# Optimization experiments

Measured on AMD Instinct MI355X. Metric: run time of the kernel, lower is better.

The kernel has to match this reference:

```python
import jax, jax.numpy as jnp
import numpy as np
from jax import lax

B, NQ, C = 2, 1024, 2048
H, DH = 16, 128
G, CD = 4, 512          # off_grps, off_dim = C // G
LR, HR = 24, 72         # low-res grid side, high-res grid side
INTER = 64
K = LR * LR             # sampled K/V tokens (grid_size == lr_size)


def setup_inputs() -> dict:
    key = jax.random.key(0)
    ks = jax.random.split(key, 16)
    s = 0.02
    d = {}
    d['hidden_states'] = jax.random.normal(ks[0], (B, NQ, C), jnp.float32)
    d['image_hd'] = jax.random.normal(ks[1], (B, HR * HR, C), jnp.float32)
    d['wq'] = jax.random.normal(ks[2], (C, C), jnp.float32) * s
    d['wk'] = jax.random.normal(ks[3], (C, C), jnp.float32) * s
    d['wv'] = jax.random.normal(ks[4], (C, C), jnp.float32) * s
    d['wo'] = jax.random.normal(ks[5], (C, C), jnp.float32) * s
    d['conv_dw_w'] = jax.random.normal(ks[6], (CD, 1, 3, 3), jnp.float32) * s
    d['ln1_w'] = jnp.ones((CD,), jnp.float32)
    d['ln1_b'] = jnp.zeros((CD,), jnp.float32)
    d['conv_lr_proj_w'] = jax.random.normal(ks[7], (INTER, CD), jnp.float32) * s
    d['proj_int_w'] = jax.random.normal(ks[8], (INTER, CD), jnp.float32) * s
    d['proj_int_b'] = jnp.zeros((INTER,), jnp.float32)
    d['ln2_w'] = jnp.ones((INTER,), jnp.float32)
    d['ln2_b'] = jnp.zeros((INTER,), jnp.float32)
    d['conv_off_w'] = jax.random.normal(ks[9], (2, INTER), jnp.float32) * s
    d['k_hd_w'] = jax.random.normal(ks[10], (C, C), jnp.float32) * s
    d['k_hd_b'] = jnp.zeros((C,), jnp.float32)
    d['v_hd_w'] = jax.random.normal(ks[11], (C, C), jnp.float32) * s
    d['v_hd_b'] = jnp.zeros((C,), jnp.float32)
    return d


def _ln_channels(x, w, b, eps=1e-5):
    # LayerNorm2d: normalize over channel axis of [N, C, H, W]
    mu = jnp.mean(x, axis=1, keepdims=True)
    var = jnp.var(x, axis=1, keepdims=True)
    xn = (x - mu) * lax.rsqrt(var + eps)
    return xn * w[None, :, None, None] + b[None, :, None, None]


def _tokens_to_grid(x, S):
    # [B, S*S, C] -> [B*G, CD, S, S]  (group channels like einops '(b) (h w) (g c) -> (b g) c h w')
    return x.reshape(B, S, S, G, CD).transpose(0, 3, 4, 1, 2).reshape(B * G, CD, S, S)


def _bilinear_sample(img, grid):
    # img [N, C, Hh, Wh]; grid [N, K, 2] (x, y) normalized to [-1, 1], align_corners=True
    N, Cc, Hh, Wh = img.shape
    x = (grid[..., 0] + 1.0) * 0.5 * (Wh - 1)
    y = (grid[..., 1] + 1.0) * 0.5 * (Hh - 1)
    x0f, y0f = jnp.floor(x), jnp.floor(y)
    wx = (x - x0f)[:, None, :]
    wy = (y - y0f)[:, None, :]
    x0 = jnp.clip(x0f.astype(jnp.int32), 0, Wh - 1)
    x1 = jnp.clip(x0 + 1, 0, Wh - 1)
    y0 = jnp.clip(y0f.astype(jnp.int32), 0, Hh - 1)
    y1 = jnp.clip(y0 + 1, 0, Hh - 1)
    imgf = img.reshape(N, Cc, Hh * Wh)
    gather = jax.vmap(lambda im, ix: im[:, ix])  # ([C,HW],[K]) -> [C,K]
    v00 = gather(imgf, y0 * Wh + x0)
    v01 = gather(imgf, y0 * Wh + x1)
    v10 = gather(imgf, y1 * Wh + x0)
    v11 = gather(imgf, y1 * Wh + x1)
    return (v00 * (1 - wx) * (1 - wy) + v01 * wx * (1 - wy)
            + v10 * (1 - wx) * wy + v11 * wx * wy)  # [N, C, K]


def _ref_grid():
    # normalized reference points as in _grid_generate (centers / (S-1) * 2 - 1)
    yy = (jnp.linspace(0.5, LR - 0.5, LR) / (LR - 1.0)) * 2.0 - 1.0
    xx = (jnp.linspace(0.5, LR - 0.5, LR) / (LR - 1.0)) * 2.0 - 1.0
    gy, gx = jnp.meshgrid(yy, xx, indexing='ij')
    return jnp.stack([gx, gy], axis=-1).reshape(K, 2)  # (x, y)


def reference(hidden_states, image_hd, wq, wk, wv, wo, conv_dw_w, ln1_w, ln1_b,
              conv_lr_proj_w, proj_int_w, proj_int_b, ln2_w, ln2_b, conv_off_w,
              k_hd_w, k_hd_b, v_hd_w, v_hd_b):
    # ---- QKV on the full sequence ----
    q = hidden_states @ wq.T
    k_txt = hidden_states @ wk.T
    v_txt = hidden_states @ wv.T

    # ---- offset network on LR image tokens (first LR*LR tokens) ----
    lr = _tokens_to_grid(hidden_states[:, :K, :], LR)          # [B*G, CD, LR, LR]
    x = lax.conv_general_dilated(lr, conv_dw_w, (1, 1), 'SAME',
                                 feature_group_count=CD,
                                 dimension_numbers=('NCHW', 'OIHW', 'NCHW'))
    x = jax.nn.silu(x)
    x = _ln_channels(x, ln1_w, ln1_b)
    x = jnp.einsum('nchw,oc->nohw', x, conv_lr_proj_w)          # 1x1 conv -> [B*G, INTER, LR, LR]
    # intention gate from spatially pooled group features
    pooled = jnp.mean(lr, axis=(2, 3))                          # [B*G, CD]
    gate = jax.nn.sigmoid(pooled @ proj_int_w.T + proj_int_b)   # [B*G, INTER]
    x = x * gate[:, :, None, None]
    x = _ln_channels(x, ln2_w, ln2_b)
    off = jnp.einsum('nchw,oc->nohw', x, conv_off_w)            # [B*G, 2, LR, LR]
    off = off.transpose(0, 2, 3, 1).reshape(B * G, K, 2)        # (x, y)
    pos = jnp.tanh(_ref_grid()[None] + off)                     # sampling locs in [-1, 1]

    # ---- deformable gather from HD features ----
    hd = _tokens_to_grid(image_hd, HR)                          # [B*G, CD, HR, HR]
    samp = _bilinear_sample(hd, pos)                            # [B*G, CD, K]
    samp = samp.reshape(B, G, CD, K).transpose(0, 3, 1, 2).reshape(B, K, C)
    k_hd = samp @ k_hd_w.T + k_hd_b
    v_hd = samp @ v_hd_w.T + v_hd_b

    # ---- attention: causal over text tokens, HD tokens fully visible ----
    k_all = jnp.concatenate([k_txt, k_hd], axis=1)              # [B, NQ+K, C]
    v_all = jnp.concatenate([v_txt, v_hd], axis=1)
    qh = q.reshape(B, NQ, H, DH).transpose(0, 2, 1, 3)
    kh = k_all.reshape(B, NQ + K, H, DH).transpose(0, 2, 1, 3)
    vh = v_all.reshape(B, NQ + K, H, DH).transpose(0, 2, 1, 3)
    scores = jnp.einsum('bhqd,bhkd->bhqk', qh, kh) / jnp.sqrt(jnp.float32(DH))
    col = jnp.arange(NQ + K)
    row = jnp.arange(NQ)
    allow = (col[None, :] >= NQ) | (col[None, :] <= row[:, None])
    scores = jnp.where(allow[None, None], scores, jnp.float32(-1e9))
    attn = jax.nn.softmax(scores, axis=-1)
    out = jnp.einsum('bhqk,bhkd->bhqd', attn, vh)
    out = out.transpose(0, 2, 1, 3).reshape(B, NQ, C)
    return out @ wo.T
```

## Files before the change

kernel.cpp:

```cpp
#include <hip/hip_runtime.h>

typedef unsigned short u16;
typedef unsigned int u32;
typedef __attribute__((ext_vector_type(8))) short bf8;
typedef __attribute__((ext_vector_type(4))) float f4;
typedef __attribute__((ext_vector_type(4))) unsigned short us4;

constexpr int B = 2;
constexpr int NQ = 1024;
constexpr int C = 2048;
constexpr int DH = 128;
constexpr int G = 4;
constexpr int CD = 512;
constexpr int LR = 24;
constexpr int HR = 72;
constexpr int INTER = 64;
constexpr int K = LR * LR;
constexpr int NKV = NQ + K;

#define MFMA16(a, b, c) __builtin_amdgcn_mfma_f32_16x16x32_bf16(a, b, c, 0, 0, 0)
#define GLDS(g, l)                                                         \
  __builtin_amdgcn_global_load_lds(                                        \
      (const __attribute__((address_space(1))) void*)(g),                  \
      (__attribute__((address_space(3))) void*)(l), 16, 0, 0)
#define SB()                               \
  do {                                     \
    __builtin_amdgcn_sched_barrier(0);     \
    __builtin_amdgcn_s_barrier();          \
    __builtin_amdgcn_sched_barrier(0);     \
  } while (0)
#define WVM(n)                                              \
  do {                                                      \
    asm volatile("s_waitcnt vmcnt(" #n ")" ::: "memory");   \
    __builtin_amdgcn_sched_barrier(0);                      \
  } while (0)

__device__ __forceinline__ u16 f2bf1(float f) {
  u32 u = __float_as_uint(f);
  u32 r = (u + 0x7fffu + ((u >> 16) & 1u)) >> 16;
  return (u16)r;
}

__global__ __launch_bounds__(256) void f2bf_k9b(
    const float* __restrict__ s0, const float* __restrict__ s1,
    const float* __restrict__ s2, const float* __restrict__ s3,
    const float* __restrict__ s4, const float* __restrict__ s5,
    const float* __restrict__ s6, const float* __restrict__ plrw,
    const float* __restrict__ cdw, u16* __restrict__ d0, u16* __restrict__ d1,
    u16* __restrict__ d2, u16* __restrict__ d3, u16* __restrict__ d4,
    u16* __restrict__ d5, u16* __restrict__ d6, float* __restrict__ wt,
    float* __restrict__ x1, float* __restrict__ pooled) {
  __shared__ float SH[16 * 577];
  const int y = blockIdx.y;
  const int t = threadIdx.x;
  if (y == 7) {
    if (blockIdx.x >= 128) return;
    const int idx = blockIdx.x * 256 + t;
    wt[idx] = plrw[(idx & 63) * 512 + (idx >> 6)];
    return;
  }
  if (y == 8) {
    if (blockIdx.x >= 256) return;
    const int n = blockIdx.x >> 5, cg = blockIdx.x & 31;
    const int b = n >> 2, g = n & 3;
    const int c0 = cg * 16;
    {
      const int c = t & 15, pr = t >> 4;
      const float* src = s0 + (size_t)b * 1024 * 2048 + g * 512 + c0 + c;
#pragma unroll 4
      for (int j = 0; j < 36; ++j) {
        const int p = j * 16 + pr;
        SH[c * 577 + p] = src[(size_t)p * 2048];
      }
    }
    __syncthreads();
    {
      const int c = t >> 4, seg = t & 15;
      float s = 0.f;
      for (int i = 0; i < 36; ++i) s += SH[c * 577 + seg * 36 + i];
      s += __shfl_xor(s, 1);
      s += __shfl_xor(s, 2);
      s += __shfl_xor(s, 4);
      s += __shfl_xor(s, 8);
      if (seg == 0) pooled[n * 512 + c0 + c] = s * (1.f / 576.f);
    }
    const size_t base_out = (size_t)(n * 512 + c0) * 576;
    for (int j = 0; j < 36; ++j) {
      const int idx = j * 256 + t;
      const int c = idx / 576, p = idx - c * 576;
      const int yy0 = p / 24, xx0 = p - yy0 * 24;
      const float* wp = cdw + (c0 + c) * 9;
      float s = 0.f;
#pragma unroll
      for (int dy = -1; dy <= 1; ++dy)
#pragma unroll
        for (int dx = -1; dx <= 1; ++dx) {
          const int yy = yy0 + dy, xx = xx0 + dx;
          if (yy < 0 || yy >= 24 || xx < 0 || xx >= 24) continue;
          s += SH[c * 577 + yy * 24 + xx] * wp[(dy + 1) * 3 + dx + 1];
        }
      x1[base_out + idx] = s / (1.f + expf(-s));
    }
    return;
  }
  const float* s;
  u16* d;
  switch (y) {
    case 0: s = s0; d = d0; break;
    case 1: s = s1; d = d1; break;
    case 2: s = s2; d = d2; break;
    case 3: s = s3; d = d3; break;
    case 4: s = s4; d = d4; break;
    case 5: s = s5; d = d5; break;
    default: s = s6; d = d6; break;
  }
  u16* L = (u16*)SH;
  const int pc = blockIdx.x;
  const int mb = pc >> 5, kb = pc & 31;
  const int rin = t >> 2, c0 = (t & 3) * 16;
  const float* src = s + (size_t)(mb * 64 + rin) * 2048 + kb * 64 + c0;
#pragma unroll
  for (int j = 0; j < 16; j += 4) {
    float4 v = *(const float4*)(src + j);
    L[rin * 68 + c0 + j] = f2bf1(v.x);
    L[rin * 68 + c0 + j + 1] = f2bf1(v.y);
    L[rin * 68 + c0 + j + 2] = f2bf1(v.z);
    L[rin * 68 + c0 + j + 3] = f2bf1(v.w);
  }
  __syncthreads();
  u16* dst = d + (size_t)pc * 4096 + t * 16;
#pragma unroll
  for (int gg = 0; gg < 2; ++gg) {
    const int g = t * 2 + gg;
    const int rh = g & 15, ks2 = (g >> 4) & 3, kc = (g >> 6) & 1, fr = g >> 7;
    const int row = fr * 16 + rh, cc = kc * 32 + ks2 * 8;
    us4 o0, o1;
    o0.x = L[row * 68 + cc];     o0.y = L[row * 68 + cc + 1];
    o0.z = L[row * 68 + cc + 2]; o0.w = L[row * 68 + cc + 3];
    o1.x = L[row * 68 + cc + 4]; o1.y = L[row * 68 + cc + 5];
    o1.z = L[row * 68 + cc + 6]; o1.w = L[row * 68 + cc + 7];
    *(us4*)(dst + gg * 8) = o0;
    *(us4*)(dst + gg * 8 + 4) = o1;
  }
}

__global__ __launch_bounds__(512, 2) void gemm_qkv_hd(
    const u16* __restrict__ Ast, const u16* __restrict__ Wq,
    const u16* __restrict__ Wk, const u16* __restrict__ Wv,
    const u16* __restrict__ sampst, const u16* __restrict__ khwst,
    const u16* __restrict__ vhwst, const float* __restrict__ khb,
    const float* __restrict__ vhb, u16* __restrict__ outq,
    u16* __restrict__ kg, u16* __restrict__ vg) {
  __shared__ u16 As[2][4][4096];
  __shared__ u16 Bs[2][4][4096];
  const int tid = threadIdx.x, lane = tid & 63, w = tid >> 6;
  const int ks = lane >> 4, r = lane & 15;
  const int bid = blockIdx.x;

  if (bid < 192) {
    const int wm = w >> 2, wn = w & 3;
    const int swz = (bid & 7) * 24 + (bid >> 3);
    const int mt = swz / 24, nt = swz % 24;
    const u16* Wst = (nt < 8) ? Wq : (nt < 16) ? Wk : Wv;
    const int nb0 = (nt & 7) * 4;
    const int mb0 = mt * 4;

#define ST_A03(bi, kt)                                                        \
  do {                                                                        \
    GLDS(Ast + ((size_t)(mb0 + 0) * 32 + (kt)) * 4096 + tid * 8,              \
         &As[bi][0][tid * 8]);                                                \
    GLDS(Ast + ((size_t)(mb0 + 2) * 32 + (kt)) * 4096 + tid * 8,              \
         &As[bi][2][tid * 8]);                                                \
  } while (0)
#define ST_A47(bi, kt)                                                        \
  do {                                                                        \
    GLDS(Ast + ((size_t)(mb0 + 1) * 32 + (kt)) * 4096 + tid * 8,              \
         &As[bi][1][tid * 8]);                                                \
    GLDS(Ast + ((size_t)(mb0 + 3) * 32 + (kt)) * 4096 + tid * 8,              \
         &As[bi][3][tid * 8]);                                                \
  } while (0)
#define ST_B01(bi, kt)                                                        \
  do {                                                                        \
    GLDS(Wst + ((size_t)(nb0 + 0) * 32 + (kt)) * 4096 + tid * 8,              \
         &Bs[bi][0][tid * 8]);                                                \
    GLDS(Wst + ((size_t)(nb0 + 1) * 32 + (kt)) * 4096 + tid * 8,              \
         &Bs[bi][1][tid * 8]);                                                \
  } while (0)
#define ST_B23(bi, kt)                                                        \
  do {                                                                        \
    GLDS(Wst + ((size_t)(nb0 + 2) * 32 + (kt)) * 4096 + tid * 8,              \
         &Bs[bi][2][tid * 8]);                                                \
    GLDS(Wst + ((size_t)(nb0 + 3) * 32 + (kt)) * 4096 + tid * 8,              \
         &Bs[bi][3][tid * 8]);                                                \
  } while (0)
#define RD_A(dst, bi, half, kc)                                               \
  _Pragma("unroll") for (int i2 = 0; i2 < 4; ++i2) dst[i2] =                  \
      *(const bf8*)(&As[bi][wm * 2 + (half)]                                  \
                       [((i2 * 2 + (kc)) * 4 + ks) * 128 + r * 8]);
#define RD_B(dst, bi, kc)                                                     \
  _Pragma("unroll") for (int j2 = 0; j2 < 4; ++j2) dst[j2] =                  \
      *(const bf8*)(&Bs[bi][wn][((j2 * 2 + (kc)) * 4 + ks) * 128 + r * 8]);
#define MM(ACC, AF, BF)                                                       \
  do {                                                                        \
    __builtin_amdgcn_s_setprio(1);                                            \
    _Pragma("unroll") for (int i3 = 0; i3 < 4; ++i3)                          \
        _Pragma("unroll") for (int j3 = 0; j3 < 4; ++j3) ACC[i3][j3] =        \
            MFMA16(AF[i3], BF[j3], ACC[i3][j3]);                              \
    __builtin_amdgcn_s_setprio(0);                                            \
  } while (0)

    f4 accA[4][4], accB[4][4];
#pragma unroll
    for (int i = 0; i < 4; ++i)
#pragma unroll
      for (int j = 0; j < 4; ++j) {
        accA[i][j] = f4{0.f, 0.f, 0.f, 0.f};
        accB[i][j] = f4{0.f, 0.f, 0.f, 0.f};
      }
    bf8 af[4], b0[4], b1[4];

    ST_A03(0, 0); ST_B01(0, 0); ST_B23(0, 0); ST_A47(0, 0);
    ST_A03(1, 1); ST_B01(1, 1);
    WVM(6);
    SB();

    for (int t = 0; t < 32; ++t) {
      const int buf = t & 1;
      RD_A(af, buf, 0, 0);
      RD_B(b0, buf, 0);
      if (t + 1 < 32) ST_B23(buf ^ 1, t + 1);
      SB();
      MM(accA, af, b0);
      SB();
      RD_A(af, buf, 0, 1);
      RD_B(b1, buf, 1);
      if (t + 1 < 32) ST_A47(buf ^ 1, t + 1);
      SB();
      MM(accA, af, b1);
      if (t + 1 < 32) { WVM(8); } else { WVM(0); }
      SB();
      RD_A(af, buf, 1, 0);
      if (t + 2 < 32) ST_A03(buf, t + 2);
      SB();
      MM(accB, af, b0);
      SB();
      RD_A(af, buf, 1, 1);
      if (t + 2 < 32) ST_B01(buf, t + 2);
      SB();
      MM(accB, af, b1);
      if (t + 2 < 32) { WVM(6); } else if (t + 1 < 32) { WVM(2); }
      SB();
    }

#define EPI(ACC, HALF)                                                        \
  _Pragma("unroll") for (int i = 0; i < 4; ++i)                               \
      _Pragma("unroll") for (int j = 0; j < 4; ++j)                           \
          _Pragma("unroll") for (int rr = 0; rr < 4; ++rr) {                  \
    const int m = mt * 256 + wm * 128 + (HALF)*64 + i * 16 + ks * 4 + rr;     \
    const int n = nt * 256 + wn * 64 + j * 16 + r;                            \
    const float v = ACC[i][j][rr];                                            \
    const int sel = n >> 11, nn = n & 2047, hh = nn >> 7, dd = nn & 127;      \
    const int bb = m >> 10, qq = m & 1023;                                    \
    const u16 bv = f2bf1(v);                                                  \
    if (sel == 0) {                                                           \
      outq[(size_t)m * 2048 + nn] = bv;                                       \
    } else if (sel == 1) {                                                    \
      kg[(((size_t)(bb * 16 + hh) * 50 + (qq >> 5)) * 16 + (dd >> 3)) * 256 + \
         (qq & 31) * 8 + (dd & 7)] = bv;                                      \
    } else {                                                                  \
      vg[((size_t)(bb * 16 + hh) * 200 + (qq >> 3)) * 1024 + dd * 8 +         \
         (qq & 7)] = bv;                                                      \
    }                                                                         \
  }
    EPI(accA, 0)
    EPI(accB, 1)
#undef EPI
  } else {
    u16* A3 = &As[0][0][0];
    u16* Bk3 = &As[0][0][0] + 12288;
    u16* Bv3 = &Bs[0][0][0];
    const int hb = bid - 192;
    const int mt = hb / 16, nt = hb % 16;
    const int ma0 = mt * 2, nb0 = nt * 2;
    const bool is_v = (w >= 4);
    const int wv4 = w & 3;
    const int wr = wv4 >> 1, wc = wv4 & 1;
    const u16* Wsrc = is_v ? vhwst : khwst;
    u16* Wdst = is_v ? Bv3 : Bk3;
    const u16* Brd = is_v ? Bv3 : Bk3;

#define HDST(bi, kt)                                                          \
  do {                                                                        \
    const int kb_ = (kt) >> 1, kc_ = (kt) & 1;                                \
    GLDS(sampst + ((size_t)(ma0 + (w >> 2)) * 32 + kb_) * 4096 +              \
             (w & 3) * 1024 + kc_ * 512 + lane * 8,                           \
         &A3[(bi)*4096 + w * 512 + lane * 8]);                                \
    _Pragma("unroll") for (int r2 = 0; r2 < 2; ++r2) {                        \
      const int run = r2 * 4 + wv4;                                           \
      GLDS(Wsrc + ((size_t)(nb0 + (run >> 2)) * 32 + kb_) * 4096 +            \
               (run & 3) * 1024 + kc_ * 512 + lane * 8,                       \
           &Wdst[(bi)*4096 + run * 512 + lane * 8]);                          \
    }                                                                         \
  } while (0)

    f4 acc[4][4];
#pragma unroll
    for (int i = 0; i < 4; ++i)
#pragma unroll
      for (int j = 0; j < 4; ++j) acc[i][j] = f4{0.f, 0.f, 0.f, 0.f};

    HDST(0, 0);
    HDST(1, 1);
    int rd = 0;
    for (int kt = 0; kt < 64; ++kt) {
      SB();
      if (kt + 2 < 64) {
        const int wb = (rd + 2 >= 3) ? rd - 1 : rd + 2;
        HDST(wb, kt + 2);
        WVM(6);
      } else if (kt + 1 < 64) {
        WVM(3);
      } else {
        WVM(0);
      }
      SB();
      bf8 af2[4], bw[4];
#pragma unroll
      for (int i = 0; i < 4; ++i)
        af2[i] =
            *(const bf8*)(&A3[rd * 4096 + (wr * 4 + i) * 512 + ks * 128 + r * 8]);
#pragma unroll
      for (int j = 0; j < 4; ++j)
        bw[j] =
            *(const bf8*)(&Brd[rd * 4096 + (wc * 4 + j) * 512 + ks * 128 + r * 8]);
      __builtin_amdgcn_s_setprio(1);
#pragma unroll
      for (int i = 0; i < 4; ++i)
#pragma unroll
        for (int j = 0; j < 4; ++j)
          acc[i][j] = MFMA16(af2[i], bw[j], acc[i][j]);
      __builtin_amdgcn_s_setprio(0);
      rd = (rd + 1 >= 3) ? 0 : rd + 1;
    }
#undef HDST
    const int rbase = ks * 4;
    const float* bias = is_v ? vhb : khb;
#pragma unroll
    for (int i = 0; i < 4; ++i)
#pragma unroll
      for (int j = 0; j < 4; ++j) {
        const int nn = nt * 128 + wc * 64 + j * 16 + r;
        const int hh = nn >> 7, dd = nn & 127;
#pragma unroll
        for (int rr = 0; rr < 4; ++rr) {
          const int m = mt * 128 + wr * 64 + i * 16 + rbase + rr;
          const int bb = m / 576;
          const int kv = 1024 + (m - bb * 576);
          const u16 bv = f2bf1(acc[i][j][rr] + bias[nn]);
          if (!is_v) {
            kg[(((size_t)(bb * 16 + hh) * 50 + (kv >> 5)) * 16 + (dd >> 3)) *
                   256 +
               (kv & 31) * 8 + (dd & 7)] = bv;
          } else {
            vg[((size_t)(bb * 16 + hh) * 200 + (kv >> 3)) * 1024 + dd * 8 +
               (kv & 7)] = bv;
          }
        }
      }
  }
}

__global__ __launch_bounds__(256) void gemm_out3(const u16* __restrict__ Ast,
                                                 const u16* __restrict__ W0,
                                                 float* __restrict__ outf) {
  __shared__ u16 As[3][4096];
  __shared__ u16 Bs[3][4096];
  const int tid = threadIdx.x, lane = tid & 63, w = tid >> 6;
  const int wr = w >> 1, wc = w & 1;
  const int ksl = lane >> 4, rl = lane & 15;
  const int xcd = blockIdx.x & 7, idx = blockIdx.x >> 3;
  const int mt = (xcd >> 2) * 8 + idx / 4;
  const int nt = (xcd & 3) * 4 + idx % 4;
  const u16* Wp = W0;
  const int ma0 = mt * 2;
  const int nb0 = nt * 2;

#define GST2(dstArr, srcBase, tb0, kt)                                     \
  do {                                                                     \
    const int kb_ = (kt) >> 1, kc_ = (kt) & 1;                             \
    _Pragma("unroll") for (int r2 = 0; r2 < 2; ++r2) {                     \
      const int run = r2 * 4 + w;                                          \
      GLDS(srcBase + ((size_t)((tb0) + (run >> 2)) * 32 + kb_) * 4096 +    \
               (run & 3) * 1024 + kc_ * 512 + lane * 8,                    \
           &dstArr[run * 512 + lane * 8]);                                 \
    }                                                                      \
  } while (0)

  f4 acc[4][4];
#pragma unroll
  for (int i = 0; i < 4; ++i)
#pragma unroll
    for (int j = 0; j < 4; ++j) acc[i][j] = f4{0.f, 0.f, 0.f, 0.f};

  GST2(As[0], Ast, ma0, 0);
  GST2(Bs[0], Wp, nb0, 0);
  GST2(As[1], Ast, ma0, 1);
  GST2(Bs[1], Wp, nb0, 1);
  int rd = 0;
  for (int kt = 0; kt < 64; ++kt) {
    SB();
    if (kt + 2 < 64) {
      const int wb = (rd + 2 >= 3) ? rd - 1 : rd + 2;
      GST2(As[wb], Ast, ma0, kt + 2);
      GST2(Bs[wb], Wp, nb0, kt + 2);
      WVM(8);
    } else if (kt + 1 < 64) {
      WVM(4);
    } else {
      WVM(0);
    }
    SB();
    bf8 af[4], bw[4];
#pragma unroll
    for (int i = 0; i < 4; ++i)
      af[i] = *(const bf8*)(&As[rd][(wr * 4 + i) * 512 + ksl * 128 + rl * 8]);
#pragma unroll
    for (int j = 0; j < 4; ++j)
      bw[j] = *(const bf8*)(&Bs[rd][(wc * 4 + j) * 512 + ksl * 128 + rl * 8]);
    __builtin_amdgcn_s_setprio(1);
#pragma unroll
    for (int i = 0; i < 4; ++i)
#pragma unroll
      for (int j = 0; j < 4; ++j)
        acc[i][j] = MFMA16(af[i], bw[j], acc[i][j]);
    __builtin_amdgcn_s_setprio(0);
    rd = (rd + 1 >= 3) ? 0 : rd + 1;
  }
#undef GST2

  const int rbase = ksl * 4;
#pragma unroll
  for (int i = 0; i < 4; ++i)
#pragma unroll
    for (int j = 0; j < 4; ++j) {
      const int n = nt * 128 + wc * 64 + j * 16 + rl;
#pragma unroll
      for (int rr = 0; rr < 4; ++rr) {
        const int m = mt * 128 + wr * 64 + i * 16 + rbase + rr;
        outf[(size_t)m * 2048 + n] = acc[i][j][rr];
      }
    }
}

__global__ __launch_bounds__(256) void lnproj_gate(
    const float* __restrict__ x1, const float* __restrict__ ln1w,
    const float* __restrict__ ln1b, const float* __restrict__ wt,
    const float* __restrict__ pooled, const float* __restrict__ piw,
    const float* __restrict__ pib, float* __restrict__ x2,
    float* __restrict__ gate) {
  __shared__ float Xs[512][68];
  __shared__ float rs[4][64], rss[4][64];
  const int bidx = blockIdx.x;
  const int t = threadIdx.x;
  if (bidx >= 72) {
    const int idx = (bidx - 72) * 256 + t;
    const int n = idx >> 6, o = idx & 63;
    const float* pb = pooled + n * 512;
    const float* wb = piw + o * 512;
    float s = pib[o];
    for (int c = 0; c < 512; ++c) s += pb[c] * wb[c];
    gate[idx] = 1.f / (1.f + expf(-s));
    return;
  }
  const int n = bidx / 9, pc = bidx % 9;
  const int p0 = pc * 64;
  {
    const int pl = t & 63, c4 = t >> 6;
    const float* src = x1 + (size_t)n * 512 * 576 + p0 + pl;
#pragma unroll 4
    for (int j = 0; j < 128; ++j) {
      const int c = j * 4 + c4;
      Xs[c][pl] = src[(size_t)c * 576];
    }
  }
  __syncthreads();
  {
    const int pl = t & 63, q = t >> 6;
    float s = 0.f, ss = 0.f;
    for (int c = q * 128; c < q * 128 + 128; ++c) {
      const float v = Xs[c][pl];
      s += v;
      ss += v * v;
    }
    rs[q][pl] = s;
    rss[q][pl] = ss;
    __syncthreads();
    const float S = rs[0][pl] + rs[1][pl] + rs[2][pl] + rs[3][pl];
    const float SS = rss[0][pl] + rss[1][pl] + rss[2][pl] + rss[3][pl];
    const float mean = S * (1.f / 512.f);
    const float inv = rsqrtf(SS * (1.f / 512.f) - mean * mean + 1e-5f);
    for (int c = q * 128; c < q * 128 + 128; ++c)
      Xs[c][pl] = (Xs[c][pl] - mean) * inv * ln1w[c] + ln1b[c];
  }
  __syncthreads();
  {
    const int o4 = (t & 15) * 4, pl0 = (t >> 4) * 4;
    float acc[4][4] = {};
    for (int c = 0; c < 512; ++c) {
      const f4 xv = *(const f4*)(&Xs[c][pl0]);
      const f4 wv = *(const f4*)(&wt[c * 64 + o4]);
#pragma unroll
      for (int i = 0; i < 4; ++i)
#pragma unroll
        for (int j = 0; j < 4; ++j) acc[i][j] += wv[i] * xv[j];
    }
#pragma unroll
    for (int i = 0; i < 4; ++i) {
      f4 ov;
      ov[0] = acc[i][0]; ov[1] = acc[i][1];
      ov[2] = acc[i][2]; ov[3] = acc[i][3];
      *(f4*)(&x2[(size_t)(n * 64 + o4 + i) * 576 + p0 + pl0]) = ov;
    }
  }
}

__global__ __launch_bounds__(256) void pos_sample(
    const float* __restrict__ x2, const float* __restrict__ gate,
    const float* __restrict__ ln2w, const float* __restrict__ ln2b,
    const float* __restrict__ offw, const float* __restrict__ img,
    u16* __restrict__ sampst) {
  const int bk = blockIdx.x;
  const int b = bk / K, k = bk % K;
  __shared__ int s_idx[G][4];
  __shared__ float s_w[G][4];
  const int t = threadIdx.x;
  const int g = t >> 6, lane = t & 63;
  {
    const int n = b * G + g;
    float v = x2[((size_t)n * INTER + lane) * K + k] * gate[n * INTER + lane];
    float s = v, ss = v * v;
    for (int o = 32; o; o >>= 1) {
      s += __shfl_xor(s, o);
      ss += __shfl_xor(ss, o);
    }
    const float mean = s * (1.f / INTER);
    const float var = ss * (1.f / INTER) - mean * mean;
    const float xn = (v - mean) * rsqrtf(var + 1e-5f) * ln2w[lane] + ln2b[lane];
    float ox = xn * offw[lane];
    float oy = xn * offw[INTER + lane];
    for (int o = 32; o; o >>= 1) {
      ox += __shfl_xor(ox, o);
      oy += __shfl_xor(oy, o);
    }
    if (lane == 0) {
      const int yi = k / LR, xi = k % LR;
      const float rx = (xi + 0.5f) / 23.f * 2.f - 1.f;
      const float ry = (yi + 0.5f) / 23.f * 2.f - 1.f;
      const float px = tanhf(rx + ox), py = tanhf(ry + oy);
      const float x = (px + 1.f) * 0.5f * (HR - 1);
      const float y = (py + 1.f) * 0.5f * (HR - 1);
      const float x0f = floorf(x), y0f = floorf(y);
      const float wx = x - x0f, wy = y - y0f;
      const int x0 = min(max((int)x0f, 0), HR - 1);
      const int x1 = min(x0 + 1, HR - 1);
      const int y0 = min(max((int)y0f, 0), HR - 1);
      const int y1 = min(y0 + 1, HR - 1);
      s_idx[g][0] = y0 * HR + x0;
      s_idx[g][1] = y0 * HR + x1;
      s_idx[g][2] = y1 * HR + x0;
      s_idx[g][3] = y1 * HR + x1;
      s_w[g][0] = (1.f - wx) * (1.f - wy);
      s_w[g][1] = wx * (1.f - wy);
      s_w[g][2] = (1.f - wx) * wy;
      s_w[g][3] = wx * wy;
    }
  }
  __syncthreads();
  const int m = b * 576 + k;
  const int mb = m >> 6, fr = (m >> 4) & 3, r = m & 15;
  const int ch0 = t * 8;
  const int gg = ch0 >> 9;
  const float* ib = img + (size_t)b * HR * HR * C + ch0;
  float v[8];
#pragma unroll
  for (int j = 0; j < 8; ++j) v[j] = 0.f;
#pragma unroll
  for (int q = 0; q < 4; ++q) {
    const float wq_ = s_w[gg][q];
    const float* p = ib + (size_t)s_idx[gg][q] * C;
    const float4 a = *(const float4*)p;
    const float4 c = *(const float4*)(p + 4);
    v[0] += wq_ * a.x; v[1] += wq_ * a.y; v[2] += wq_ * a.z; v[3] += wq_ * a.w;
    v[4] += wq_ * c.x; v[5] += wq_ * c.y; v[6] += wq_ * c.z; v[7] += wq_ * c.w;
  }
  const int kb = ch0 >> 6, kc = (ch0 >> 5) & 1, ks3 = (ch0 >> 3) & 3;
  u16* dst = sampst + ((size_t)(mb * 32 + kb)) * 4096 +
             (((fr * 2 + kc) * 4 + ks3) * 16 + r) * 8;
  us4 o0, o1;
  o0.x = f2bf1(v[0]); o0.y = f2bf1(v[1]); o0.z = f2bf1(v[2]); o0.w = f2bf1(v[3]);
  o1.x = f2bf1(v[4]); o1.y = f2bf1(v[5]); o1.z = f2bf1(v[6]); o1.w = f2bf1(v[7]);
  *(us4*)dst = o0;
  *(us4*)(dst + 4) = o1;
}

__global__ __launch_bounds__(256) void attn_u(
    const u16* __restrict__ qb, const u16* __restrict__ kg,
    const u16* __restrict__ vg, u16* __restrict__ aob_st) {
  const int i = blockIdx.x;
  const int pair = i & 255, half = i >> 8;
  const int bh = pair & 31;
  const int q8 = pair >> 5;
  const int qblk = half ? (15 - q8) : q8;
  const int b = bh >> 4, h = bh & 15;
  const int q0 = qblk * 64;
  const int tid = threadIdx.x, lane = tid & 63, w = tid >> 6;
  const int qw = q0 + w * 16;
  const int col = lane & 15, kpart = lane >> 4, rbase = kpart * 4;
  __shared__ u16 Ks[2][4096];
  __shared__ u16 Vs[2][4096];
  __shared__ u16 Pl[4][16 * 40];
  bf8 qf[4];
  {
    const u16* qp =
        qb + (size_t)(b * 1024 + qw + col) * 2048 + h * 128 + kpart * 8;
#pragma unroll
    for (int dc = 0; dc < 4; ++dc) qf[dc] = *(const bf8*)(qp + dc * 32);
  }
  f4 o[8];
#pragma unroll
  for (int df = 0; df < 8; ++df) o[df] = f4{0.f, 0.f, 0.f, 0.f};
  float m_r[4] = {-1e30f, -1e30f, -1e30f, -1e30f};
  float l_p[4] = {0.f, 0.f, 0.f, 0.f};
  const float scale = 0.08838834764831845f;
  const int nt_text = (q0 + 64) >> 5;
  const int nt = nt_text + 18;
  const u16* kbh = kg + (size_t)bh * (NKV * 128);
  const u16* vbh = vg + (size_t)bh * (NKV * 128);
  u16* pw = &Pl[w][0];

#define ASTAGE(bi, kv0)                                                       \
  do {                                                                        \
    const u16* gk = kbh + (size_t)((kv0) >> 5) * 4096 + w * 1024 + lane * 8;  \
    GLDS(gk, &Ks[bi][w * 1024 + lane * 8]);                                   \
    GLDS(gk + 512, &Ks[bi][w * 1024 + 512 + lane * 8]);                       \
    const u16* gv = vbh + (size_t)((kv0) >> 3) * 1024 + w * 1024 + lane * 8;  \
    GLDS(gv, &Vs[bi][w * 1024 + lane * 8]);                                   \
    GLDS(gv + 512, &Vs[bi][w * 1024 + 512 + lane * 8]);                       \
  } while (0)

  ASTAGE(0, 0);
  int cur = 0;
  for (int t = 0; t < nt; ++t) {
    const bool is_text = t < nt_text;
    const int kv0 = is_text ? (t << 5) : (1024 + ((t - nt_text) << 5));
    SB();
    if (t + 1 < nt) {
      const int t1 = t + 1;
      const int kv1 =
          (t1 < nt_text) ? (t1 << 5) : (1024 + ((t1 - nt_text) << 5));
      ASTAGE(cur ^ 1, kv1);
      WVM(4);
    } else {
      WVM(0);
    }
    SB();
    const u16* ksb = &Ks[cur][0];
    const u16* vsb = &Vs[cur][0];
    f4 s0 = {0.f, 0.f, 0.f, 0.f}, s1 = {0.f, 0.f, 0.f, 0.f};
    __builtin_amdgcn_s_setprio(1);
#pragma unroll
    for (int dc = 0; dc < 4; ++dc) {
      const int dblk = dc * 4 + kpart;
      bf8 k0f = *(const bf8*)(ksb + (dblk * 32 + col) * 8);
      bf8 k1f = *(const bf8*)(ksb + (dblk * 32 + 16 + col) * 8);
      s0 = MFMA16(qf[dc], k0f, s0);
      s1 = MFMA16(qf[dc], k1f, s1);
    }
    __builtin_amdgcn_s_setprio(0);
    float sa[4], sc[4], loc[4], p0[4], p1[4];
    bool grow = false;
    const bool need_mask = is_text && (kv0 + 31 > qw);
#pragma unroll
    for (int rr = 0; rr < 4; ++rr) {
      float a = s0[rr] * scale, c2 = s1[rr] * scale;
      if (need_mask) {
        const int qg = qw + rbase + rr;
        if (kv0 + col > qg) a = -1e30f;
        if (kv0 + 16 + col > qg) c2 = -1e30f;
      }
      sa[rr] = a; sc[rr] = c2;
      loc[rr] = fmaxf(a, c2);
      grow |= (loc[rr] > m_r[rr] + 8.f);
    }
    if (__any(grow)) {
      float fr[4];
#pragma unroll
      for (int rr = 0; rr < 4; ++rr) {
        float mx = loc[rr];
        mx = fmaxf(mx, __shfl_xor(mx, 1));
        mx = fmaxf(mx, __shfl_xor(mx, 2));
        mx = fmaxf(mx, __shfl_xor(mx, 4));
        mx = fmaxf(mx, __shfl_xor(mx, 8));
        const float mn = fmaxf(m_r[rr], mx);
        fr[rr] = __expf(m_r[rr] - mn);
        m_r[rr] = mn;
        p0[rr] = __expf(sa[rr] - mn);
        p1[rr] = __expf(sc[rr] - mn);
        l_p[rr] = l_p[rr] * fr[rr] + p0[rr] + p1[rr];
      }
#pragma unroll
      for (int df = 0; df < 8; ++df) {
        o[df][0] *= fr[0]; o[df][1] *= fr[1];
        o[df][2] *= fr[2]; o[df][3] *= fr[3];
      }
    } else {
#pragma unroll
      for (int rr = 0; rr < 4; ++rr) {
        p0[rr] = __expf(sa[rr] - m_r[rr]);
        p1[rr] = __expf(sc[rr] - m_r[rr]);
        l_p[rr] += p0[rr] + p1[rr];
      }
    }
#pragma unroll
    for (int rr = 0; rr < 4; ++rr) {
      pw[(rbase + rr) * 40 + col] = f2bf1(p0[rr]);
      pw[(rbase + rr) * 40 + 16 + col] = f2bf1(p1[rr]);
    }
    bf8 pa = *(const bf8*)(pw + col * 40 + kpart * 8);
    __builtin_amdgcn_s_setprio(1);
#pragma unroll
    for (int df = 0; df < 8; ++df) {
      bf8 vf = *(const bf8*)(vsb + (kpart * 128 + df * 16 + col) * 8);
      o[df] = MFMA16(pa, vf, o[df]);
    }
    __builtin_amdgcn_s_setprio(0);
    cur ^= 1;
  }
#undef ASTAGE
  float inv[4];
#pragma unroll
  for (int rr = 0; rr < 4; ++rr) {
    float ps = l_p[rr];
    ps += __shfl_xor(ps, 1);
    ps += __shfl_xor(ps, 2);
    ps += __shfl_xor(ps, 4);
    ps += __shfl_xor(ps, 8);
    inv[rr] = 1.f / ps;
  }
#pragma unroll
  for (int rr = 0; rr < 4; ++rr) {
    const int m = b * 1024 + qw + rbase + rr;
    const int mb = m >> 6, fr3 = (m >> 4) & 3, r16 = m & 15;
#pragma unroll
    for (int df = 0; df < 8; ++df) {
      const int ncol = h * 128 + df * 16 + col;
      const int kb = ncol >> 6, kc = (ncol >> 5) & 1, ks3 = (ncol >> 3) & 3,
                j0 = ncol & 7;
      aob_st[((size_t)(mb * 32 + kb)) * 4096 +
             (((fr3 * 2 + kc) * 4 + ks3) * 16 + r16) * 8 + j0] =
          f2bf1(o[df][rr] * inv[rr]);
    }
  }
}

extern "C" void kernel_launch(void* const* d_in, const int* in_sizes, int n_in,
                              void* d_out, int out_size, void* d_ws,
                              size_t ws_size, hipStream_t stream) {
  const float* hs = (const float*)d_in[0];
  const float* img = (const float*)d_in[1];
  const float* wq = (const float*)d_in[2];
  const float* wk = (const float*)d_in[3];
  const float* wv = (const float*)d_in[4];
  const float* wo = (const float*)d_in[5];
  const float* cdw = (const float*)d_in[6];
  const float* ln1w = (const float*)d_in[7];
  const float* ln1b = (const float*)d_in[8];
  const float* plrw = (const float*)d_in[9];
  const float* piw = (const float*)d_in[10];
  const float* pib = (const float*)d_in[11];
  const float* ln2w = (const float*)d_in[12];
  const float* ln2b = (const float*)d_in[13];
  const float* offw = (const float*)d_in[14];
  const float* khw = (const float*)d_in[15];
  const float* khb = (const float*)d_in[16];
  const float* vhw = (const float*)d_in[17];
  const float* vhb = (const float*)d_in[18];
  float* outp = (float*)d_out;

  u16* wsp = (u16*)d_ws;
  const size_t SZ = 4194304;
  u16* hs_st = wsp;
  u16* wq_st = wsp + SZ;
  u16* wk_st = wsp + 2 * SZ;
  u16* wv_st = wsp + 3 * SZ;
  u16* wo_st = wsp + 4 * SZ;
  u16* khw_st = wsp + 5 * SZ;
  u16* vhw_st = wsp + 6 * SZ;
  u16* qb_bf = wsp + 7 * SZ;
  u16* samp_st = wsp + 8 * SZ;
  u16* kg = wsp + 8 * SZ + 2359296;
  u16* vg = kg + 6553600;
  float* x1b = (float*)kg + 2359296;
  float* x2b = x1b + 2359296;
  float* poolb = x2b + 294912;
  float* gb = poolb + 4096;
  float* wtb = (float*)(vg + 6553600);
  u16* aob_st = wq_st;

  dim3 blk(256);
  f2bf_k9b<<<dim3(1024, 9), blk, 0, stream>>>(
      hs, wq, wk, wv, wo, khw, vhw, plrw, cdw, hs_st, wq_st, wk_st, wv_st,
      wo_st, khw_st, vhw_st, wtb, x1b, poolb);
  lnproj_gate<<<dim3(74), blk, 0, stream>>>(x1b, ln1w, ln1b, wtb, poolb, piw,
                                            pib, x2b, gb);
  pos_sample<<<dim3(B * K), blk, 0, stream>>>(x2b, gb, ln2w, ln2b, offw, img,
                                              samp_st);
  gemm_qkv_hd<<<dim3(336), dim3(512), 0, stream>>>(
      hs_st, wq_st, wk_st, wv_st, samp_st, khw_st, vhw_st, khb, vhb, qb_bf,
      kg, vg);
  attn_u<<<dim3(512), blk, 0, stream>>>(qb_bf, kg, vg, aob_st);
  gemm_out3<<<dim3(256), blk, 0, stream>>>(aob_st, wo_st, outp);
}
```

Baseline: 338.0 us.

## Widen attention KV tile to 64 keys and reorder QKV/HD GEMM block dispatch

The attention kernel now processes 64 keys per pipeline step instead of 32. This halves the number of barrier and stage iterations and the softmax bookkeeping per key, at the cost of doubled LDS buffers and more registers. Separately, the fused GEMM kernel now assigns the low block IDs to the HD sampled-token K/V blocks and the later IDs to the Q/K/V projection blocks. This changes which work is scheduled first, likely to let the longer HD blocks start earlier.

```diff
diff --git a/kernel.cpp b/kernel.cpp
--- a/kernel.cpp
+++ b/kernel.cpp
@@ -157,9 +157,10 @@
   const int ks = lane >> 4, r = lane & 15;
   const int bid = blockIdx.x;
 
-  if (bid < 192) {
+  if (bid >= 144) {
+    const int qbid = bid - 144;
     const int wm = w >> 2, wn = w & 3;
-    const int swz = (bid & 7) * 24 + (bid >> 3);
+    const int swz = (qbid & 7) * 24 + (qbid >> 3);
     const int mt = swz / 24, nt = swz % 24;
     const u16* Wst = (nt < 8) ? Wq : (nt < 16) ? Wk : Wv;
     const int nb0 = (nt & 7) * 4;
@@ -279,7 +280,7 @@
     u16* A3 = &As[0][0][0];
     u16* Bk3 = &As[0][0][0] + 12288;
     u16* Bv3 = &Bs[0][0][0];
-    const int hb = bid - 192;
+    const int hb = bid;
     const int mt = hb / 16, nt = hb % 16;
     const int ma0 = mt * 2, nb0 = nt * 2;
     const bool is_v = (w >= 4);
@@ -603,7 +604,7 @@
   *(us4*)(dst + 4) = o1;
 }
 
-__global__ __launch_bounds__(256) void attn_u(
+__global__ __launch_bounds__(256) void attn_u64(
     const u16* __restrict__ qb, const u16* __restrict__ kg,
     const u16* __restrict__ vg, u16* __restrict__ aob_st) {
   const int i = blockIdx.x;
@@ -616,9 +617,9 @@
   const int tid = threadIdx.x, lane = tid & 63, w = tid >> 6;
   const int qw = q0 + w * 16;
   const int col = lane & 15, kpart = lane >> 4, rbase = kpart * 4;
-  __shared__ u16 Ks[2][4096];
-  __shared__ u16 Vs[2][4096];
-  __shared__ u16 Pl[4][16 * 40];
+  __shared__ u16 Ks[2][8192];
+  __shared__ u16 Vs[2][8192];
+  __shared__ u16 Pl[4][16 * 72];
   bf8 qf[4];
   {
     const u16* qp =
@@ -632,34 +633,38 @@
   float m_r[4] = {-1e30f, -1e30f, -1e30f, -1e30f};
   float l_p[4] = {0.f, 0.f, 0.f, 0.f};
   const float scale = 0.08838834764831845f;
-  const int nt_text = (q0 + 64) >> 5;
-  const int nt = nt_text + 18;
+  const int nt_text = qblk + 1;
+  const int nt = nt_text + 9;
   const u16* kbh = kg + (size_t)bh * (NKV * 128);
   const u16* vbh = vg + (size_t)bh * (NKV * 128);
   u16* pw = &Pl[w][0];
 
-#define ASTAGE(bi, kv0)                                                       \
+#define ASTG64(bi, kv0)                                                       \
   do {                                                                        \
-    const u16* gk = kbh + (size_t)((kv0) >> 5) * 4096 + w * 1024 + lane * 8;  \
-    GLDS(gk, &Ks[bi][w * 1024 + lane * 8]);                                   \
-    GLDS(gk + 512, &Ks[bi][w * 1024 + 512 + lane * 8]);                       \
-    const u16* gv = vbh + (size_t)((kv0) >> 3) * 1024 + w * 1024 + lane * 8;  \
-    GLDS(gv, &Vs[bi][w * 1024 + lane * 8]);                                   \
-    GLDS(gv + 512, &Vs[bi][w * 1024 + 512 + lane * 8]);                       \
-  } while (0)
-
-  ASTAGE(0, 0);
+    const u16* gk = kbh + (size_t)((kv0) >> 5) * 4096 + w * 2048 + lane * 8;  \
+    GLDS(gk, &Ks[bi][w * 2048 + lane * 8]);                                   \
+    GLDS(gk + 512, &Ks[bi][w * 2048 + 512 + lane * 8]);                       \
+    GLDS(gk + 1024, &Ks[bi][w * 2048 + 1024 + lane * 8]);                     \
+    GLDS(gk + 1536, &Ks[bi][w * 2048 + 1536 + lane * 8]);                     \
+    const u16* gv = vbh + (size_t)((kv0) >> 3) * 1024 + w * 2048 + lane * 8;  \
+    GLDS(gv, &Vs[bi][w * 2048 + lane * 8]);                                   \
+    GLDS(gv + 512, &Vs[bi][w * 2048 + 512 + lane * 8]);                       \
+    GLDS(gv + 1024, &Vs[bi][w * 2048 + 1024 + lane * 8]);                     \
+    GLDS(gv + 1536, &Vs[bi][w * 2048 + 1536 + lane * 8]);                     \
+  } while (0)
+
+  ASTG64(0, 0);
   int cur = 0;
   for (int t = 0; t < nt; ++t) {
     const bool is_text = t < nt_text;
-    const int kv0 = is_text ? (t << 5) : (1024 + ((t - nt_text) << 5));
+    const int kv0 = is_text ? (t << 6) : (1024 + ((t - nt_text) << 6));
     SB();
     if (t + 1 < nt) {
       const int t1 = t + 1;
       const int kv1 =
-          (t1 < nt_text) ? (t1 << 5) : (1024 + ((t1 - nt_text) << 5));
-      ASTAGE(cur ^ 1, kv1);
-      WVM(4);
+          (t1 < nt_text) ? (t1 << 6) : (1024 + ((t1 - nt_text) << 6));
+      ASTG64(cur ^ 1, kv1);
+      WVM(8);
     } else {
       WVM(0);
     }
@@ -667,29 +672,37 @@
     const u16* ksb = &Ks[cur][0];
     const u16* vsb = &Vs[cur][0];
     f4 s0 = {0.f, 0.f, 0.f, 0.f}, s1 = {0.f, 0.f, 0.f, 0.f};
+    f4 s2 = {0.f, 0.f, 0.f, 0.f}, s3 = {0.f, 0.f, 0.f, 0.f};
     __builtin_amdgcn_s_setprio(1);
 #pragma unroll
     for (int dc = 0; dc < 4; ++dc) {
       const int dblk = dc * 4 + kpart;
       bf8 k0f = *(const bf8*)(ksb + (dblk * 32 + col) * 8);
       bf8 k1f = *(const bf8*)(ksb + (dblk * 32 + 16 + col) * 8);
+      bf8 k2f = *(const bf8*)(ksb + 4096 + (dblk * 32 + col) * 8);
+      bf8 k3f = *(const bf8*)(ksb + 4096 + (dblk * 32 + 16 + col) * 8);
       s0 = MFMA16(qf[dc], k0f, s0);
       s1 = MFMA16(qf[dc], k1f, s1);
+      s2 = MFMA16(qf[dc], k2f, s2);
+      s3 = MFMA16(qf[dc], k3f, s3);
     }
     __builtin_amdgcn_s_setprio(0);
-    float sa[4], sc[4], loc[4], p0[4], p1[4];
+    float sa[4][4], loc[4], p[4][4];
     bool grow = false;
-    const bool need_mask = is_text && (kv0 + 31 > qw);
+    const bool need_mask = is_text && (kv0 + 63 > qw);
 #pragma unroll
     for (int rr = 0; rr < 4; ++rr) {
-      float a = s0[rr] * scale, c2 = s1[rr] * scale;
+      float a0 = s0[rr] * scale, a1 = s1[rr] * scale;
+      float a2 = s2[rr] * scale, a3 = s3[rr] * scale;
       if (need_mask) {
         const int qg = qw + rbase + rr;
-        if (kv0 + col > qg) a = -1e30f;
-        if (kv0 + 16 + col > qg) c2 = -1e30f;
+        if (kv0 + col > qg) a0 = -1e30f;
+        if (kv0 + 16 + col > qg) a1 = -1e30f;
+        if (kv0 + 32 + col > qg) a2 = -1e30f;
+        if (kv0 + 48 + col > qg) a3 = -1e30f;
       }
-      sa[rr] = a; sc[rr] = c2;
-      loc[rr] = fmaxf(a, c2);
+      sa[rr][0] = a0; sa[rr][1] = a1; sa[rr][2] = a2; sa[rr][3] = a3;
+      loc[rr] = fmaxf(fmaxf(a0, a1), fmaxf(a2, a3));
       grow |= (loc[rr] > m_r[rr] + 8.f);
     }
     if (__any(grow)) {
@@ -704,9 +717,9 @@
         const float mn = fmaxf(m_r[rr], mx);
         fr[rr] = __expf(m_r[rr] - mn);
         m_r[rr] = mn;
-        p0[rr] = __expf(sa[rr] - mn);
-        p1[rr] = __expf(sc[rr] - mn);
-        l_p[rr] = l_p[rr] * fr[rr] + p0[rr] + p1[rr];
+#pragma unroll
+        for (int jj = 0; jj < 4; ++jj) p[rr][jj] = __expf(sa[rr][jj] - mn);
+        l_p[rr] = l_p[rr] * fr[rr] + p[rr][0] + p[rr][1] + p[rr][2] + p[rr][3];
       }
 #pragma unroll
       for (int df = 0; df < 8; ++df) {
@@ -716,27 +729,32 @@
     } else {
 #pragma unroll
       for (int rr = 0; rr < 4; ++rr) {
-        p0[rr] = __expf(sa[rr] - m_r[rr]);
-        p1[rr] = __expf(sc[rr] - m_r[rr]);
-        l_p[rr] += p0[rr] + p1[rr];
+#pragma unroll
+        for (int jj = 0; jj < 4; ++jj) p[rr][jj] = __expf(sa[rr][jj] - m_r[rr]);
+        l_p[rr] += p[rr][0] + p[rr][1] + p[rr][2] + p[rr][3];
       }
     }
 #pragma unroll
     for (int rr = 0; rr < 4; ++rr) {
-      pw[(rbase + rr) * 40 + col] = f2bf1(p0[rr]);
-      pw[(rbase + rr) * 40 + 16 + col] = f2bf1(p1[rr]);
-    }
-    bf8 pa = *(const bf8*)(pw + col * 40 + kpart * 8);
+      pw[(rbase + rr) * 72 + col] = f2bf1(p[rr][0]);
+      pw[(rbase + rr) * 72 + 16 + col] = f2bf1(p[rr][1]);
+      pw[(rbase + rr) * 72 + 32 + col] = f2bf1(p[rr][2]);
+      pw[(rbase + rr) * 72 + 48 + col] = f2bf1(p[rr][3]);
+    }
+    bf8 pa0 = *(const bf8*)(pw + col * 72 + kpart * 8);
+    bf8 pa1 = *(const bf8*)(pw + col * 72 + 32 + kpart * 8);
     __builtin_amdgcn_s_setprio(1);
 #pragma unroll
     for (int df = 0; df < 8; ++df) {
-      bf8 vf = *(const bf8*)(vsb + (kpart * 128 + df * 16 + col) * 8);
-      o[df] = MFMA16(pa, vf, o[df]);
+      bf8 vf0 = *(const bf8*)(vsb + (kpart * 128 + df * 16 + col) * 8);
+      bf8 vf1 = *(const bf8*)(vsb + ((kpart + 4) * 128 + df * 16 + col) * 8);
+      o[df] = MFMA16(pa0, vf0, o[df]);
+      o[df] = MFMA16(pa1, vf1, o[df]);
     }
     __builtin_amdgcn_s_setprio(0);
     cur ^= 1;
   }
-#undef ASTAGE
+#undef ASTG64
   float inv[4];
 #pragma unroll
   for (int rr = 0; rr < 4; ++rr) {
@@ -818,6 +836,6 @@
   gemm_qkv_hd<<<dim3(336), dim3(512), 0, stream>>>(
       hs_st, wq_st, wk_st, wv_st, samp_st, khw_st, vhw_st, khb, vhb, qb_bf,
       kg, vg);
-  attn_u<<<dim3(512), blk, 0, stream>>>(qb_bf, kg, vg, aob_st);
+  attn_u64<<<dim3(512), blk, 0, stream>>>(qb_bf, kg, vg, aob_st);
   gemm_out3<<<dim3(256), blk, 0, stream>>>(aob_st, wo_st, outp);
 }
```

Result: no change. 338.5 us (+0.1%).
